# Optimization experiments

Measured on AMD Instinct MI355X. Metric: run time of the kernel, lower is better.

Reference implementation:

```python
import jax, jax.numpy as jnp
import numpy as np

B, K, D = 128, 2048, 512   # batch, out_features (classes), in_features
C = 1.0                    # curvature c


def setup_inputs() -> dict:
    key = jax.random.key(0)
    k1, k2, k3 = jax.random.split(key, 3)
    # inputs must lie strictly inside the Poincare ball of radius 1/sqrt(c)
    v = jax.random.normal(k1, (B, D), jnp.float32)
    inp = v * (0.7 / (1.0 + jnp.linalg.norm(v, axis=-1, keepdims=True)))
    # p is a hyperbolic parameter (init zeros in the module; use small in-ball
    # values here so the math is non-degenerate)
    pv = jax.random.normal(k2, (K, D), jnp.float32)
    p = pv * (0.3 / (1.0 + jnp.linalg.norm(pv, axis=-1, keepdims=True)))
    # a is Euclidean, xavier-uniform scale ~ 1/sqrt(D)
    a = jax.random.normal(k3, (K, D), jnp.float32) * (1.0 / np.sqrt(D))
    return {"inp": inp, "p": p, "a": a}


def hyperbolic_logits(inp, p, a, c):
    """Ganea et al. hyperbolic MLR logits.

    logit_k(x) = (lambda_{p_k} ||a_k|| / sqrt(c))
                 * asinh( 2 sqrt(c) <(-p_k) (+)_c x, a_k>
                          / ((1 - c ||(-p_k)(+)_c x||^2) ||a_k||) )
    """
    c = jnp.float32(c)
    sc = jnp.sqrt(c)
    u = -p                                   # [K,D]
    uv = jnp.einsum('bd,kd->bk', inp, u)     # <u_k, x_b>
    uu = jnp.sum(u * u, -1)                  # [K]
    vv = jnp.sum(inp * inp, -1)              # [B]
    # Mobius addition w = u (+)_c x, broadcast to [B,K,D]
    alpha = 1.0 + 2.0 * c * uv + c * vv[:, None]          # coeff of u
    beta = 1.0 - c * uu[None, :]                           # coeff of x
    den = 1.0 + 2.0 * c * uv + (c * c) * uu[None, :] * vv[:, None]
    w = (alpha[..., None] * u[None, :, :]
         + beta[..., None] * inp[:, None, :]) / den[..., None]   # [B,K,D]
    ww = jnp.sum(w * w, -1)                  # [B,K]
    wa = jnp.einsum('bkd,kd->bk', w, a)      # [B,K]
    a_norm = jnp.linalg.norm(a, axis=-1)     # [K]
    lam_p = 2.0 / (1.0 - c * jnp.sum(p * p, -1))   # conformal factor at p_k
    num = 2.0 * sc * wa
    denom = a_norm[None, :] * (1.0 - c * ww)
    return (lam_p * a_norm / sc)[None, :] * jnp.arcsinh(num / denom)  # [B,K]


def reference(inp, p, a):
    return hyperbolic_logits(inp, p, a, C)
```

## Files before the change

### kernel.cpp

```cpp
#include <hip/hip_runtime.h>

#define B_SZ 128
#define K_SZ 2048
#define D_SZ 512
#define ROWP 520

typedef __attribute__((ext_vector_type(8))) short short8;
typedef __attribute__((ext_vector_type(4))) float floatx4;

static __device__ inline unsigned short f2b(float f) {
  __bf16 h = (__bf16)f;
  return __builtin_bit_cast(unsigned short, h);
}

__global__ __launch_bounds__(256, 2) void fused_kernel(
    const float* __restrict__ x, const float* __restrict__ p,
    const float* __restrict__ a, float* __restrict__ out) {
  __shared__ unsigned short xs[32 * ROWP];
  __shared__ unsigned short ps[16 * ROWP];
  __shared__ unsigned short as_[16 * ROWP];
  __shared__ float stats[32 + 48];

  const int t = threadIdx.x;
  const int bm = (blockIdx.x >> 7) * 32;
  const int kn = (blockIdx.x & 127) * 16;

  {
    const int r = t >> 3, s = t & 7;
    const float4* src = (const float4*)(x + (size_t)(bm + r) * D_SZ);
    float vvp = 0.f;
#pragma unroll
    for (int i = 0; i < 16; ++i) {
      float4 v = src[s + i * 8];
      vvp += v.x * v.x + v.y * v.y + v.z * v.z + v.w * v.w;
      ushort4 c;
      c.x = f2b(v.x); c.y = f2b(v.y); c.z = f2b(v.z); c.w = f2b(v.w);
      *(ushort4*)&xs[r * ROWP + (s + i * 8) * 4] = c;
    }
    vvp += __shfl_xor(vvp, 1, 64);
    vvp += __shfl_xor(vvp, 2, 64);
    vvp += __shfl_xor(vvp, 4, 64);
    if (s == 0) stats[r] = vvp;
  }

  {
    const int r = t >> 4, s = t & 15;
    const float4* sp = (const float4*)(p + (size_t)(kn + r) * D_SZ);
    const float4* sa = (const float4*)(a + (size_t)(kn + r) * D_SZ);
    float pp = 0.f, pa = 0.f, aa = 0.f;
#pragma unroll
    for (int i = 0; i < 8; ++i) {
      float4 pv = sp[s + i * 16];
      float4 av = sa[s + i * 16];
      pp += pv.x * pv.x + pv.y * pv.y + pv.z * pv.z + pv.w * pv.w;
      pa += pv.x * av.x + pv.y * av.y + pv.z * av.z + pv.w * av.w;
      aa += av.x * av.x + av.y * av.y + av.z * av.z + av.w * av.w;
      ushort4 pc, ac;
      pc.x = f2b(pv.x); pc.y = f2b(pv.y); pc.z = f2b(pv.z); pc.w = f2b(pv.w);
      ac.x = f2b(av.x); ac.y = f2b(av.y); ac.z = f2b(av.z); ac.w = f2b(av.w);
      *(ushort4*)&ps[r * ROWP + (s + i * 16) * 4] = pc;
      *(ushort4*)&as_[r * ROWP + (s + i * 16) * 4] = ac;
    }
    pp += __shfl_xor(pp, 1, 64);
    pa += __shfl_xor(pa, 1, 64);
    aa += __shfl_xor(aa, 1, 64);
    pp += __shfl_xor(pp, 2, 64);
    pa += __shfl_xor(pa, 2, 64);
    aa += __shfl_xor(aa, 2, 64);
    pp += __shfl_xor(pp, 4, 64);
    pa += __shfl_xor(pa, 4, 64);
    aa += __shfl_xor(aa, 4, 64);
    pp += __shfl_xor(pp, 8, 64);
    pa += __shfl_xor(pa, 8, 64);
    aa += __shfl_xor(aa, 8, 64);
    if (s == 0) {
      stats[32 + r] = pp;
      stats[48 + r] = -pa;
      stats[64 + r] = sqrtf(aa);
    }
  }
  __syncthreads();

  const int w = t >> 6, lane = t & 63;
  const int row16 = lane & 15, quad = lane >> 4;
  const int wm = w & 1, dh = w >> 1;
  const unsigned short* xrow = &xs[(wm * 16 + row16) * ROWP + dh * 256 + quad * 8];
  const unsigned short* prow = &ps[row16 * ROWP + dh * 256 + quad * 8];
  const unsigned short* arow = &as_[row16 * ROWP + dh * 256 + quad * 8];
  floatx4 cs = {0.f, 0.f, 0.f, 0.f};
  floatx4 ca = {0.f, 0.f, 0.f, 0.f};
#pragma unroll
  for (int dc = 0; dc < 8; ++dc) {
    short8 af = *(const short8*)(xrow + dc * 32);
    short8 bp = *(const short8*)(prow + dc * 32);
    short8 bv = *(const short8*)(arow + dc * 32);
    cs = __builtin_amdgcn_mfma_f32_16x16x32_bf16(af, bp, cs, 0, 0, 0);
    ca = __builtin_amdgcn_mfma_f32_16x16x32_bf16(af, bv, ca, 0, 0, 0);
  }

  __syncthreads();
  float* part_s = (float*)ps;
  float* part_a = part_s + 1024;
  *(floatx4*)&part_s[(w * 64 + lane) * 4] = cs;
  *(floatx4*)&part_a[(w * 64 + lane) * 4] = ca;
  __syncthreads();

#pragma unroll
  for (int o = 0; o < 2; ++o) {
    const int idx = t + o * 256;
    const int m16 = idx >> 4;
    const int n = idx & 15;
    const int wmI = m16 >> 4, mr = m16 & 15;
    const int lsrc = ((mr >> 2) << 4) | n;
    const int reg = mr & 3;
    const float sdot = part_s[(wmI * 64 + lsrc) * 4 + reg] +
                       part_s[((2 + wmI) * 64 + lsrc) * 4 + reg];
    const float adot = part_a[(wmI * 64 + lsrc) * 4 + reg] +
                       part_a[((2 + wmI) * 64 + lsrc) * 4 + reg];
    const float vvb = stats[m16];
    const float uuk = stats[32 + n];
    const float nuak = stats[48 + n];
    const float ank = stats[64 + n];
    const float beta = 1.f - uuk;
    const float scale = (2.f / beta) * ank;
    const float uv = -sdot;
    const float alpha = 1.f + 2.f * uv + vvb;
    const float den = 1.f + 2.f * uv + uuk * vvb;
    const float inv = 1.f / den;
    const float wwn =
        (alpha * alpha * uuk + 2.f * alpha * beta * uv + beta * beta * vvb) *
        inv * inv;
    const float wa = (alpha * nuak + beta * adot) * inv;
    const float z = 2.f * wa / (ank * (1.f - wwn));
    out[(size_t)(bm + m16) * K_SZ + (kn + n)] = scale * asinhf(z);
  }
}

extern "C" void kernel_launch(void* const* d_in, const int* in_sizes, int n_in,
                              void* d_out, int out_size, void* d_ws, size_t ws_size,
                              hipStream_t stream) {
  const float* x = (const float*)d_in[0];
  const float* p = (const float*)d_in[1];
  const float* a = (const float*)d_in[2];
  float* out = (float*)d_out;
  (void)d_ws; (void)ws_size;

  fused_kernel<<<(B_SZ / 32) * (K_SZ / 16), 256, 0, stream>>>(x, p, a, out);
}
```

Measured before the change: 66.66 us.

## Load MFMA operands directly from global memory, skipping LDS staging

The kernel no longer converts x, p and a tiles into bf16 in shared memory. Each wave now loads its own D-slice straight from global memory into registers, converts it there and feeds the MFMAs, computing the norm and dot statistics along the way. The reduction is split four ways over D, one slice per wave, and the partial sums are combined through a smaller shared buffer. This removes the LDS write/read round trip and one barrier, and lowers shared-memory use so more blocks can be resident. In exchange the global loads are strided per lane, which may coalesce less well, and the final reduction reads four partials instead of two.

```diff
diff --git a/kernel.cpp b/kernel.cpp
--- a/kernel.cpp
+++ b/kernel.cpp
@@ -3,7 +3,6 @@
 #define B_SZ 128
 #define K_SZ 2048
 #define D_SZ 512
-#define ROWP 520
 
 typedef __attribute__((ext_vector_type(8))) short short8;
 typedef __attribute__((ext_vector_type(4))) float floatx4;
@@ -13,98 +12,94 @@
   return __builtin_bit_cast(unsigned short, h);
 }
 
-__global__ __launch_bounds__(256, 2) void fused_kernel(
+static __device__ inline short8 cvt8(float4 lo, float4 hi) {
+  short8 r;
+  r[0] = (short)f2b(lo.x); r[1] = (short)f2b(lo.y);
+  r[2] = (short)f2b(lo.z); r[3] = (short)f2b(lo.w);
+  r[4] = (short)f2b(hi.x); r[5] = (short)f2b(hi.y);
+  r[6] = (short)f2b(hi.z); r[7] = (short)f2b(hi.w);
+  return r;
+}
+
+__global__ __launch_bounds__(256) void fused_kernel(
     const float* __restrict__ x, const float* __restrict__ p,
     const float* __restrict__ a, float* __restrict__ out) {
-  __shared__ unsigned short xs[32 * ROWP];
-  __shared__ unsigned short ps[16 * ROWP];
-  __shared__ unsigned short as_[16 * ROWP];
-  __shared__ float stats[32 + 48];
+  __shared__ float lds[4416];
 
   const int t = threadIdx.x;
-  const int bm = (blockIdx.x >> 7) * 32;
-  const int kn = (blockIdx.x & 127) * 16;
+  const int mt = blockIdx.x >> 7;
+  const int kt = blockIdx.x & 127;
+  const int w = t >> 6, lane = t & 63;
+  const int row16 = lane & 15, quad = lane >> 4;
 
-  {
-    const int r = t >> 3, s = t & 7;
-    const float4* src = (const float4*)(x + (size_t)(bm + r) * D_SZ);
-    float vvp = 0.f;
+  const int dbase = w * 128 + quad * 8;
+  const float* xb0 = x + (size_t)(mt * 32 + row16) * D_SZ + dbase;
+  const float* xb1 = xb0 + (size_t)16 * D_SZ;
+  const float* pbr = p + (size_t)(kt * 16 + row16) * D_SZ + dbase;
+  const float* abr = a + (size_t)(kt * 16 + row16) * D_SZ + dbase;
+
+  floatx4 cs0 = {0.f, 0.f, 0.f, 0.f}, cs1 = {0.f, 0.f, 0.f, 0.f};
+  floatx4 ca0 = {0.f, 0.f, 0.f, 0.f}, ca1 = {0.f, 0.f, 0.f, 0.f};
+  float vv0 = 0.f, vv1 = 0.f, pp = 0.f, pa = 0.f, aa = 0.f;
+
 #pragma unroll
-    for (int i = 0; i < 16; ++i) {
-      float4 v = src[s + i * 8];
-      vvp += v.x * v.x + v.y * v.y + v.z * v.z + v.w * v.w;
-      ushort4 c;
-      c.x = f2b(v.x); c.y = f2b(v.y); c.z = f2b(v.z); c.w = f2b(v.w);
-      *(ushort4*)&xs[r * ROWP + (s + i * 8) * 4] = c;
-    }
-    vvp += __shfl_xor(vvp, 1, 64);
-    vvp += __shfl_xor(vvp, 2, 64);
-    vvp += __shfl_xor(vvp, 4, 64);
-    if (s == 0) stats[r] = vvp;
+  for (int dc = 0; dc < 4; ++dc) {
+    const int off = dc * 32;
+    float4 x00 = *(const float4*)(xb0 + off);
+    float4 x01 = *(const float4*)(xb0 + off + 4);
+    float4 x10 = *(const float4*)(xb1 + off);
+    float4 x11 = *(const float4*)(xb1 + off + 4);
+    float4 pv0 = *(const float4*)(pbr + off);
+    float4 pv1 = *(const float4*)(pbr + off + 4);
+    float4 av0 = *(const float4*)(abr + off);
+    float4 av1 = *(const float4*)(abr + off + 4);
+
+    vv0 += x00.x * x00.x + x00.y * x00.y + x00.z * x00.z + x00.w * x00.w +
+           x01.x * x01.x + x01.y * x01.y + x01.z * x01.z + x01.w * x01.w;
+    vv1 += x10.x * x10.x + x10.y * x10.y + x10.z * x10.z + x10.w * x10.w +
+           x11.x * x11.x + x11.y * x11.y + x11.z * x11.z + x11.w * x11.w;
+    pp += pv0.x * pv0.x + pv0.y * pv0.y + pv0.z * pv0.z + pv0.w * pv0.w +
+          pv1.x * pv1.x + pv1.y * pv1.y + pv1.z * pv1.z + pv1.w * pv1.w;
+    pa += pv0.x * av0.x + pv0.y * av0.y + pv0.z * av0.z + pv0.w * av0.w +
+          pv1.x * av1.x + pv1.y * av1.y + pv1.z * av1.z + pv1.w * av1.w;
+    aa += av0.x * av0.x + av0.y * av0.y + av0.z * av0.z + av0.w * av0.w +
+          av1.x * av1.x + av1.y * av1.y + av1.z * av1.z + av1.w * av1.w;
+
+    short8 af0 = cvt8(x00, x01);
+    short8 af1 = cvt8(x10, x11);
+    short8 bp = cvt8(pv0, pv1);
+    short8 bv = cvt8(av0, av1);
+    cs0 = __builtin_amdgcn_mfma_f32_16x16x32_bf16(af0, bp, cs0, 0, 0, 0);
+    cs1 = __builtin_amdgcn_mfma_f32_16x16x32_bf16(af1, bp, cs1, 0, 0, 0);
+    ca0 = __builtin_amdgcn_mfma_f32_16x16x32_bf16(af0, bv, ca0, 0, 0, 0);
+    ca1 = __builtin_amdgcn_mfma_f32_16x16x32_bf16(af1, bv, ca1, 0, 0, 0);
   }
 
-  {
-    const int r = t >> 4, s = t & 15;
-    const float4* sp = (const float4*)(p + (size_t)(kn + r) * D_SZ);
-    const float4* sa = (const float4*)(a + (size_t)(kn + r) * D_SZ);
-    float pp = 0.f, pa = 0.f, aa = 0.f;
-#pragma unroll
-    for (int i = 0; i < 8; ++i) {
-      float4 pv = sp[s + i * 16];
-      float4 av = sa[s + i * 16];
-      pp += pv.x * pv.x + pv.y * pv.y + pv.z * pv.z + pv.w * pv.w;
-      pa += pv.x * av.x + pv.y * av.y + pv.z * av.z + pv.w * av.w;
-      aa += av.x * av.x + av.y * av.y + av.z * av.z + av.w * av.w;
-      ushort4 pc, ac;
-      pc.x = f2b(pv.x); pc.y = f2b(pv.y); pc.z = f2b(pv.z); pc.w = f2b(pv.w);
-      ac.x = f2b(av.x); ac.y = f2b(av.y); ac.z = f2b(av.z); ac.w = f2b(av.w);
-      *(ushort4*)&ps[r * ROWP + (s + i * 16) * 4] = pc;
-      *(ushort4*)&as_[r * ROWP + (s + i * 16) * 4] = ac;
-    }
-    pp += __shfl_xor(pp, 1, 64);
-    pa += __shfl_xor(pa, 1, 64);
-    aa += __shfl_xor(aa, 1, 64);
-    pp += __shfl_xor(pp, 2, 64);
-    pa += __shfl_xor(pa, 2, 64);
-    aa += __shfl_xor(aa, 2, 64);
-    pp += __shfl_xor(pp, 4, 64);
-    pa += __shfl_xor(pa, 4, 64);
-    aa += __shfl_xor(aa, 4, 64);
-    pp += __shfl_xor(pp, 8, 64);
-    pa += __shfl_xor(pa, 8, 64);
-    aa += __shfl_xor(aa, 8, 64);
-    if (s == 0) {
-      stats[32 + r] = pp;
-      stats[48 + r] = -pa;
-      stats[64 + r] = sqrtf(aa);
-    }
-  }
+  vv0 += __shfl_xor(vv0, 16, 64); vv0 += __shfl_xor(vv0, 32, 64);
+  vv1 += __shfl_xor(vv1, 16, 64); vv1 += __shfl_xor(vv1, 32, 64);
+  pp  += __shfl_xor(pp, 16, 64);  pp  += __shfl_xor(pp, 32, 64);
+  pa  += __shfl_xor(pa, 16, 64);  pa  += __shfl_xor(pa, 32, 64);
+  aa  += __shfl_xor(aa, 16, 64);  aa  += __shfl_xor(aa, 32, 64);
+
+  float* pS0 = lds;
+  float* pS1 = lds + 1024;
+  float* pA0 = lds + 2048;
+  float* pA1 = lds + 3072;
+  float* vvL = lds + 4096;
+  float* ppL = lds + 4224;
+  float* paL = lds + 4288;
+  float* aaL = lds + 4352;
+  *(floatx4*)&pS0[t * 4] = cs0;
+  *(floatx4*)&pS1[t * 4] = cs1;
+  *(floatx4*)&pA0[t * 4] = ca0;
+  *(floatx4*)&pA1[t * 4] = ca1;
+  if (quad == 0) { vvL[row16 * 4 + w] = vv0; aaL[row16 * 4 + w] = aa; }
+  if (quad == 1) vvL[(16 + row16) * 4 + w] = vv1;
+  if (quad == 2) ppL[row16 * 4 + w] = pp;
+  if (quad == 3) paL[row16 * 4 + w] = pa;
   __syncthreads();
 
-  const int w = t >> 6, lane = t & 63;
-  const int row16 = lane & 15, quad = lane >> 4;
-  const int wm = w & 1, dh = w >> 1;
-  const unsigned short* xrow = &xs[(wm * 16 + row16) * ROWP + dh * 256 + quad * 8];
-  const unsigned short* prow = &ps[row16 * ROWP + dh * 256 + quad * 8];
-  const unsigned short* arow = &as_[row16 * ROWP + dh * 256 + quad * 8];
-  floatx4 cs = {0.f, 0.f, 0.f, 0.f};
-  floatx4 ca = {0.f, 0.f, 0.f, 0.f};
-#pragma unroll
-  for (int dc = 0; dc < 8; ++dc) {
-    short8 af = *(const short8*)(xrow + dc * 32);
-    short8 bp = *(const short8*)(prow + dc * 32);
-    short8 bv = *(const short8*)(arow + dc * 32);
-    cs = __builtin_amdgcn_mfma_f32_16x16x32_bf16(af, bp, cs, 0, 0, 0);
-    ca = __builtin_amdgcn_mfma_f32_16x16x32_bf16(af, bv, ca, 0, 0, 0);
-  }
-
-  __syncthreads();
-  float* part_s = (float*)ps;
-  float* part_a = part_s + 1024;
-  *(floatx4*)&part_s[(w * 64 + lane) * 4] = cs;
-  *(floatx4*)&part_a[(w * 64 + lane) * 4] = ca;
-  __syncthreads();
-
+  const int bm = mt * 32, kn = kt * 16;
 #pragma unroll
   for (int o = 0; o < 2; ++o) {
     const int idx = t + o * 256;
@@ -113,14 +108,20 @@
     const int wmI = m16 >> 4, mr = m16 & 15;
     const int lsrc = ((mr >> 2) << 4) | n;
     const int reg = mr & 3;
-    const float sdot = part_s[(wmI * 64 + lsrc) * 4 + reg] +
-                       part_s[((2 + wmI) * 64 + lsrc) * 4 + reg];
-    const float adot = part_a[(wmI * 64 + lsrc) * 4 + reg] +
-                       part_a[((2 + wmI) * 64 + lsrc) * 4 + reg];
-    const float vvb = stats[m16];
-    const float uuk = stats[32 + n];
-    const float nuak = stats[48 + n];
-    const float ank = stats[64 + n];
+    const float* S = wmI ? pS1 : pS0;
+    const float* A = wmI ? pA1 : pA0;
+    const float sdot = S[lsrc * 4 + reg] + S[(64 + lsrc) * 4 + reg] +
+                       S[(128 + lsrc) * 4 + reg] + S[(192 + lsrc) * 4 + reg];
+    const float adot = A[lsrc * 4 + reg] + A[(64 + lsrc) * 4 + reg] +
+                       A[(128 + lsrc) * 4 + reg] + A[(192 + lsrc) * 4 + reg];
+    floatx4 v4 = *(const floatx4*)&vvL[m16 * 4];
+    floatx4 u4 = *(const floatx4*)&ppL[n * 4];
+    floatx4 q4 = *(const floatx4*)&paL[n * 4];
+    floatx4 a4 = *(const floatx4*)&aaL[n * 4];
+    const float vvb = (v4[0] + v4[1]) + (v4[2] + v4[3]);
+    const float uuk = (u4[0] + u4[1]) + (u4[2] + u4[3]);
+    const float nuak = -((q4[0] + q4[1]) + (q4[2] + q4[3]));
+    const float ank = sqrtf((a4[0] + a4[1]) + (a4[2] + a4[3]));
     const float beta = 1.f - uuk;
     const float scale = (2.f / beta) * ank;
     const float uv = -sdot;
```

Result: slower. 70.41 us (+5.6%).
